# Performance work log

Hardware: AMD Instinct MI355X
Metric: run time of the kernel (lower is better)

The kernel has to match this reference:

```python
import jax, jax.numpy as jnp
import numpy as np

SCALE = 128.0          # GriddingDistance scale
GRID_MIN = -64.0       # floor(min coord) for points in (-64, 64)
R = 128                # voxels per axis = ceil(max) - floor(min)
G = R * R * R          # flattened grid size per sample

# 8 trilinear corner offsets (8, 3)
_CORNERS = jnp.array([[i, j, k] for i in (0, 1) for j in (0, 1) for k in (0, 1)], dtype=jnp.int32)


def _gridding(cloud):
    """Trilinear scatter of (b, n, 3) scaled points into (b, G) voxel grid.

    Mirrors gridding.forward: per point, weight each of the 8 surrounding
    voxel corners by prod(1 - |p - corner|) and scatter-add into the grid.
    """
    b, n, _ = cloud.shape
    p = cloud - GRID_MIN                     # shift to [0, R)
    x0f = jnp.floor(p)
    d = p - x0f                              # (b, n, 3) fractional offsets
    x0 = x0f.astype(jnp.int32)
    idx = jnp.clip(x0[:, :, None, :] + _CORNERS, 0, R - 1)      # (b, n, 8, 3)
    # corner weight: d for the +1 corner, (1 - d) for the base corner
    w = jnp.where(_CORNERS[None, None] == 1, d[:, :, None, :], 1.0 - d[:, :, None, :])
    w = w.prod(axis=-1)                      # (b, n, 8)
    flat = (idx[..., 0] * R + idx[..., 1]) * R + idx[..., 2]    # (b, n, 8)
    flat = flat + jnp.arange(b, dtype=jnp.int32)[:, None, None] * G
    grid = jnp.zeros(b * G, dtype=cloud.dtype).at[flat.reshape(-1)].add(w.reshape(-1))
    return grid.reshape(b, G)


def setup_inputs() -> dict:
    key = jax.random.key(0)
    k1, k2 = jax.random.split(key)
    # normalized clouds in (-0.49, 0.49) so scaled points stay inside the grid
    pred = (jax.random.uniform(k1, (8, 65536, 3), dtype=jnp.float32) - 0.5) * 0.98
    gt = (jax.random.uniform(k2, (8, 65536, 3), dtype=jnp.float32) - 0.5) * 0.98
    return {"pred_cloud": pred, "gt_cloud": gt}


def reference(pred_cloud, gt_cloud):
    pred_grid = _gridding(pred_cloud * SCALE)
    gt_grid = _gridding(gt_cloud * SCALE)
    return pred_grid, gt_grid
```

## Files before the change

### kernel.cpp

```cpp
#include <hip/hip_runtime.h>


#define RES   128
#define GRIDG (RES * RES * RES)
#define NSLAB 16
#define NREG  64
#define NBIN  (NSLAB * NREG)
#define CAPB  2048
#define PTS_PER_BLOCK 1024

__device__ __forceinline__ int clampi(int v) {
    return v < 0 ? 0 : (v > RES - 1 ? RES - 1 : v);
}


__global__ __launch_bounds__(256) void place_kernel(
    const float* __restrict__ pred, const float* __restrict__ gt,
    unsigned* __restrict__ cursor,
    float* __restrict__ bins,
    int npts, int nblkPerSlab)
{
    __shared__ unsigned cnt[NREG];
    __shared__ unsigned curs[NREG];

    const int gblk = blockIdx.x;
    const int slab = gblk / nblkPerSlab;
    const int blk  = gblk - slab * nblkPerSlab;
    const float* cloud = (slab < 8) ? pred : gt;
    const int sample = slab & 7;
    const float* cbase = cloud + (size_t)sample * npts * 3;

    if (threadIdx.x < NREG) cnt[threadIdx.x] = 0;
    __syncthreads();

    float px[4], py[4], pz[4];
    bool valid[4];

#pragma unroll
    for (int k = 0; k < 4; ++k) {
        const int j = blk * PTS_PER_BLOCK + k * 256 + threadIdx.x;
        valid[k] = (j < npts);
        if (valid[k]) {
            const float x = fmaf(cbase[(size_t)j * 3 + 0], 128.0f, 64.0f);
            const float y = fmaf(cbase[(size_t)j * 3 + 1], 128.0f, 64.0f);
            const float z = fmaf(cbase[(size_t)j * 3 + 2], 128.0f, 64.0f);
            px[k] = x; py[k] = y; pz[k] = z;
            const int ix = (int)floorf(x), iy = (int)floorf(y), iz = (int)floorf(z);
            const int rx0 = clampi(ix) >> 5, rx1 = clampi(ix + 1) >> 5;
            const int ry0 = clampi(iy) >> 5, ry1 = clampi(iy + 1) >> 5;
            const int rz0 = clampi(iz) >> 5, rz1 = clampi(iz + 1) >> 5;
            for (int a = rx0; a <= rx1; ++a)
                for (int b = ry0; b <= ry1; ++b)
                    for (int c = rz0; c <= rz1; ++c)
                        atomicAdd(&cnt[(a << 4) | (b << 2) | c], 1u);
        }
    }
    __syncthreads();

    if (threadIdx.x < NREG) {
        const unsigned c = cnt[threadIdx.x];
        unsigned base = 0;
        if (c) base = atomicAdd(&cursor[slab * NREG + threadIdx.x], c);
        curs[threadIdx.x] = base;
    }
    __syncthreads();

#pragma unroll
    for (int k = 0; k < 4; ++k) {
        if (!valid[k]) continue;
        const float x = px[k], y = py[k], z = pz[k];
        const int ix = (int)floorf(x), iy = (int)floorf(y), iz = (int)floorf(z);
        const int rx0 = clampi(ix) >> 5, rx1 = clampi(ix + 1) >> 5;
        const int ry0 = clampi(iy) >> 5, ry1 = clampi(iy + 1) >> 5;
        const int rz0 = clampi(iz) >> 5, rz1 = clampi(iz + 1) >> 5;
        for (int a = rx0; a <= rx1; ++a)
            for (int b = ry0; b <= ry1; ++b)
                for (int c = rz0; c <= rz1; ++c) {
                    const int r = (a << 4) | (b << 2) | c;
                    const unsigned slot = atomicAdd(&curs[r], 1u);
                    if (slot < CAPB) {
                        const size_t off = ((size_t)(slab * NREG + r) * CAPB + slot) * 3;
                        bins[off + 0] = x;
                        bins[off + 1] = y;
                        bins[off + 2] = z;
                    }
                }
    }
}

__global__ __launch_bounds__(1024) void accum_kernel(
    const float* __restrict__ bins, const unsigned* __restrict__ cursor,
    float* __restrict__ out)
{
    __shared__ __align__(16) float vox[32 * 32 * 32];

    const int bin  = blockIdx.x;
    const int slab = bin >> 6;
    const int reg  = bin & 63;
    const int rx = (reg >> 4) & 3, ry = (reg >> 2) & 3, rz = reg & 3;

    unsigned n = cursor[bin];
    if (n > CAPB) n = CAPB;

    for (int i = threadIdx.x; i < 32768; i += 1024) vox[i] = 0.0f;
    __syncthreads();

    const float* seg = bins + (size_t)bin * CAPB * 3;
    for (unsigned i = threadIdx.x; i < n; i += 1024) {
        const float x = seg[(size_t)i * 3 + 0];
        const float y = seg[(size_t)i * 3 + 1];
        const float z = seg[(size_t)i * 3 + 2];
        const float xf = floorf(x), yf = floorf(y), zf = floorf(z);
        const float dx = x - xf, dy = y - yf, dz = z - zf;
        const int ix = (int)xf, iy = (int)yf, iz = (int)zf;
        const int x0 = clampi(ix), x1 = clampi(ix + 1);
        const int y0 = clampi(iy), y1 = clampi(iy + 1);
        const int z0 = clampi(iz), z1 = clampi(iz + 1);
        const float wx0 = 1.0f - dx, wy0 = 1.0f - dy, wz0 = 1.0f - dz;

#pragma unroll
        for (int cc = 0; cc < 8; ++cc) {
            const int cx = (cc & 4) ? x1 : x0;
            const int cy = (cc & 2) ? y1 : y0;
            const int cz = (cc & 1) ? z1 : z0;
            if (((cx >> 5) == rx) & ((cy >> 5) == ry) & ((cz >> 5) == rz)) {
                const float w = ((cc & 4) ? dx : wx0) *
                                ((cc & 2) ? dy : wy0) *
                                ((cc & 1) ? dz : wz0);
                atomicAdd(&vox[((cx & 31) << 10) | ((cy & 31) << 5) | (cz & 31)], w);
            }
        }
    }
    __syncthreads();

    float* gp = out + (size_t)slab * GRIDG
              + ((size_t)rx << 19) + (ry << 12) + (rz << 5);
    for (int v = threadIdx.x; v < 8192; v += 1024) {
        const int l  = v << 2;
        const int lx = l >> 10, ly = (l >> 5) & 31, lz = l & 31;
        *(float4*)(gp + ((size_t)lx << 14) + (ly << 7) + lz) = *(const float4*)&vox[l];
    }
}


__global__ __launch_bounds__(256) void gridding_scatter_kernel(
    const float* __restrict__ cloud, float* __restrict__ grid, int n)
{
    const int j = blockIdx.x * blockDim.x + threadIdx.x;
    if (j >= n) return;
    const int b = blockIdx.y;
    const size_t pt = (size_t)b * n + j;

    const float x = fmaf(cloud[pt * 3 + 0], 128.0f, 64.0f);
    const float y = fmaf(cloud[pt * 3 + 1], 128.0f, 64.0f);
    const float z = fmaf(cloud[pt * 3 + 2], 128.0f, 64.0f);
    const float xf = floorf(x), yf = floorf(y), zf = floorf(z);
    const float dx = x - xf, dy = y - yf, dz = z - zf;
    const int ix = (int)xf, iy = (int)yf, iz = (int)zf;
    const int x0 = clampi(ix), x1 = clampi(ix + 1);
    const int y0 = clampi(iy), y1 = clampi(iy + 1);
    const int z0 = clampi(iz), z1 = clampi(iz + 1);
    const float wx0 = 1.0f - dx, wy0 = 1.0f - dy, wz0 = 1.0f - dz;

    float* gp = grid + (size_t)b * GRIDG;
    const int bx0 = x0 << 14, bx1 = x1 << 14;
    const int by0 = y0 << 7,  by1 = y1 << 7;
    atomicAdd(gp + (bx0 + by0 + z0), wx0 * wy0 * wz0);
    atomicAdd(gp + (bx0 + by0 + z1), wx0 * wy0 * dz);
    atomicAdd(gp + (bx0 + by1 + z0), wx0 * dy * wz0);
    atomicAdd(gp + (bx0 + by1 + z1), wx0 * dy * dz);
    atomicAdd(gp + (bx1 + by0 + z0), dx * wy0 * wz0);
    atomicAdd(gp + (bx1 + by0 + z1), dx * wy0 * dz);
    atomicAdd(gp + (bx1 + by1 + z0), dx * dy * wz0);
    atomicAdd(gp + (bx1 + by1 + z1), dx * dy * dz);
}


extern "C" void kernel_launch(void* const* d_in, const int* in_sizes, int n_in,
                              void* d_out, int out_size, void* d_ws, size_t ws_size,
                              hipStream_t stream) {
    const float* pred = (const float*)d_in[0];
    const float* gt   = (const float*)d_in[1];
    float* out = (float*)d_out;

    const int bsz  = 8;
    const int npts = in_sizes[0] / (bsz * 3);

    const size_t cursorBytes = 4096;
    const size_t binsBytes   = (size_t)NBIN * CAPB * 3 * sizeof(float);
    const size_t needWs      = cursorBytes + binsBytes;

    if (ws_size >= needWs) {
        unsigned* cursor = (unsigned*)d_ws;
        float* bins = (float*)((char*)d_ws + cursorBytes);

        hipMemsetAsync(cursor, 0, NBIN * sizeof(unsigned), stream);

        const int nblkPerSlab = (npts + PTS_PER_BLOCK - 1) / PTS_PER_BLOCK;
        place_kernel<<<dim3(NSLAB * nblkPerSlab), dim3(256), 0, stream>>>(
            pred, gt, cursor, bins, npts, nblkPerSlab);
        accum_kernel<<<dim3(NBIN), dim3(1024), 0, stream>>>(bins, cursor, out);
    } else {
        hipMemsetAsync(d_out, 0, (size_t)out_size * sizeof(float), stream);
        dim3 block(256);
        dim3 grid((npts + 255) / 256, bsz);
        float* pred_grid = out;
        float* gt_grid   = out + (size_t)bsz * GRIDG;
        gridding_scatter_kernel<<<grid, block, 0, stream>>>(pred, pred_grid, npts);
        gridding_scatter_kernel<<<grid, block, 0, stream>>>(gt,   gt_grid,   npts);
    }
}
```

Baseline: 192.9 us.

## Bin points into 16x16 xy columns with float4 records and vectorized loads

```diff
diff --git a/kernel.cpp b/kernel.cpp
--- a/kernel.cpp
+++ b/kernel.cpp
@@ -17,7 +17,7 @@
 __global__ __launch_bounds__(256) void place_kernel(
     const float* __restrict__ pred, const float* __restrict__ gt,
     unsigned* __restrict__ cursor,
-    float* __restrict__ bins,
+    float4* __restrict__ bins,
     int npts, int nblkPerSlab)
 {
     __shared__ unsigned cnt[NREG];
@@ -28,7 +28,7 @@
     const int blk  = gblk - slab * nblkPerSlab;
     const float* cloud = (slab < 8) ? pred : gt;
     const int sample = slab & 7;
-    const float* cbase = cloud + (size_t)sample * npts * 3;
+    const float* cbase = cloud + (size_t)sample * npts * 3 + (size_t)blk * PTS_PER_BLOCK * 3;
 
     if (threadIdx.x < NREG) cnt[threadIdx.x] = 0;
     __syncthreads();
@@ -36,24 +36,49 @@
     float px[4], py[4], pz[4];
     bool valid[4];
 
+    const int t = threadIdx.x;
+    const bool fullBlock = ((blk + 1) * PTS_PER_BLOCK) <= npts;
+
+    if (fullBlock) {
+        const float4* b4 = (const float4*)cbase;
+        const float4 f0 = b4[3 * t + 0];
+        const float4 f1 = b4[3 * t + 1];
+        const float4 f2 = b4[3 * t + 2];
+        px[0] = f0.x; py[0] = f0.y; pz[0] = f0.z;
+        px[1] = f0.w; py[1] = f1.x; pz[1] = f1.y;
+        px[2] = f1.z; py[2] = f1.w; pz[2] = f2.x;
+        px[3] = f2.y; py[3] = f2.z; pz[3] = f2.w;
+#pragma unroll
+        for (int k = 0; k < 4; ++k) {
+            valid[k] = true;
+            px[k] = fmaf(px[k], 128.0f, 64.0f);
+            py[k] = fmaf(py[k], 128.0f, 64.0f);
+            pz[k] = fmaf(pz[k], 128.0f, 64.0f);
+        }
+    } else {
+#pragma unroll
+        for (int k = 0; k < 4; ++k) {
+            const int j = blk * PTS_PER_BLOCK + 4 * t + k;
+            const int jj = 4 * t + k;
+            valid[k] = (blk * PTS_PER_BLOCK + jj < npts);
+            if (valid[k]) {
+                px[k] = fmaf(cbase[(size_t)jj * 3 + 0], 128.0f, 64.0f);
+                py[k] = fmaf(cbase[(size_t)jj * 3 + 1], 128.0f, 64.0f);
+                pz[k] = fmaf(cbase[(size_t)jj * 3 + 2], 128.0f, 64.0f);
+            }
+            (void)j;
+        }
+    }
+
 #pragma unroll
     for (int k = 0; k < 4; ++k) {
-        const int j = blk * PTS_PER_BLOCK + k * 256 + threadIdx.x;
-        valid[k] = (j < npts);
-        if (valid[k]) {
-            const float x = fmaf(cbase[(size_t)j * 3 + 0], 128.0f, 64.0f);
-            const float y = fmaf(cbase[(size_t)j * 3 + 1], 128.0f, 64.0f);
-            const float z = fmaf(cbase[(size_t)j * 3 + 2], 128.0f, 64.0f);
-            px[k] = x; py[k] = y; pz[k] = z;
-            const int ix = (int)floorf(x), iy = (int)floorf(y), iz = (int)floorf(z);
-            const int rx0 = clampi(ix) >> 5, rx1 = clampi(ix + 1) >> 5;
-            const int ry0 = clampi(iy) >> 5, ry1 = clampi(iy + 1) >> 5;
-            const int rz0 = clampi(iz) >> 5, rz1 = clampi(iz + 1) >> 5;
-            for (int a = rx0; a <= rx1; ++a)
-                for (int b = ry0; b <= ry1; ++b)
-                    for (int c = rz0; c <= rz1; ++c)
-                        atomicAdd(&cnt[(a << 4) | (b << 2) | c], 1u);
-        }
+        if (!valid[k]) continue;
+        const int ix = (int)floorf(px[k]), iy = (int)floorf(py[k]);
+        const int rx0 = clampi(ix) >> 4, rx1 = clampi(ix + 1) >> 4;
+        const int ry0 = clampi(iy) >> 4, ry1 = clampi(iy + 1) >> 4;
+        for (int a = rx0; a <= rx1; ++a)
+            for (int b = ry0; b <= ry1; ++b)
+                atomicAdd(&cnt[(a << 3) | b], 1u);
     }
     __syncthreads();
 
@@ -69,47 +94,43 @@
     for (int k = 0; k < 4; ++k) {
         if (!valid[k]) continue;
         const float x = px[k], y = py[k], z = pz[k];
-        const int ix = (int)floorf(x), iy = (int)floorf(y), iz = (int)floorf(z);
-        const int rx0 = clampi(ix) >> 5, rx1 = clampi(ix + 1) >> 5;
-        const int ry0 = clampi(iy) >> 5, ry1 = clampi(iy + 1) >> 5;
-        const int rz0 = clampi(iz) >> 5, rz1 = clampi(iz + 1) >> 5;
+        const int ix = (int)floorf(x), iy = (int)floorf(y);
+        const int rx0 = clampi(ix) >> 4, rx1 = clampi(ix + 1) >> 4;
+        const int ry0 = clampi(iy) >> 4, ry1 = clampi(iy + 1) >> 4;
         for (int a = rx0; a <= rx1; ++a)
-            for (int b = ry0; b <= ry1; ++b)
-                for (int c = rz0; c <= rz1; ++c) {
-                    const int r = (a << 4) | (b << 2) | c;
-                    const unsigned slot = atomicAdd(&curs[r], 1u);
-                    if (slot < CAPB) {
-                        const size_t off = ((size_t)(slab * NREG + r) * CAPB + slot) * 3;
-                        bins[off + 0] = x;
-                        bins[off + 1] = y;
-                        bins[off + 2] = z;
-                    }
+            for (int b = ry0; b <= ry1; ++b) {
+                const int r = (a << 3) | b;
+                const unsigned slot = atomicAdd(&curs[r], 1u);
+                if (slot < CAPB) {
+                    bins[(size_t)(slab * NREG + r) * CAPB + slot] =
+                        make_float4(x, y, z, 0.0f);
                 }
+            }
     }
 }
 
 __global__ __launch_bounds__(1024) void accum_kernel(
-    const float* __restrict__ bins, const unsigned* __restrict__ cursor,
+    const float4* __restrict__ bins, const unsigned* __restrict__ cursor,
     float* __restrict__ out)
 {
-    __shared__ __align__(16) float vox[32 * 32 * 32];
+    __shared__ __align__(16) float vox[16 * 16 * 128];
 
     const int bin  = blockIdx.x;
     const int slab = bin >> 6;
     const int reg  = bin & 63;
-    const int rx = (reg >> 4) & 3, ry = (reg >> 2) & 3, rz = reg & 3;
+    const int rx = reg >> 3, ry = reg & 7;
 
     unsigned n = cursor[bin];
     if (n > CAPB) n = CAPB;
 
-    for (int i = threadIdx.x; i < 32768; i += 1024) vox[i] = 0.0f;
-    __syncthreads();
-
-    const float* seg = bins + (size_t)bin * CAPB * 3;
+    float4* v4 = (float4*)vox;
+    for (int i = threadIdx.x; i < 8192; i += 1024) v4[i] = make_float4(0, 0, 0, 0);
+    __syncthreads();
+
+    const float4* seg = bins + (size_t)bin * CAPB;
     for (unsigned i = threadIdx.x; i < n; i += 1024) {
-        const float x = seg[(size_t)i * 3 + 0];
-        const float y = seg[(size_t)i * 3 + 1];
-        const float z = seg[(size_t)i * 3 + 2];
+        const float4 e = seg[i];
+        const float x = e.x, y = e.y, z = e.z;
         const float xf = floorf(x), yf = floorf(y), zf = floorf(z);
         const float dx = x - xf, dy = y - yf, dz = z - zf;
         const int ix = (int)xf, iy = (int)yf, iz = (int)zf;
@@ -119,26 +140,29 @@
         const float wx0 = 1.0f - dx, wy0 = 1.0f - dy, wz0 = 1.0f - dz;
 
 #pragma unroll
-        for (int cc = 0; cc < 8; ++cc) {
-            const int cx = (cc & 4) ? x1 : x0;
-            const int cy = (cc & 2) ? y1 : y0;
-            const int cz = (cc & 1) ? z1 : z0;
-            if (((cx >> 5) == rx) & ((cy >> 5) == ry) & ((cz >> 5) == rz)) {
-                const float w = ((cc & 4) ? dx : wx0) *
-                                ((cc & 2) ? dy : wy0) *
-                                ((cc & 1) ? dz : wz0);
-                atomicAdd(&vox[((cx & 31) << 10) | ((cy & 31) << 5) | (cz & 31)], w);
+        for (int sx = 0; sx < 2; ++sx) {
+            const int cx = sx ? x1 : x0;
+            if ((cx >> 4) != rx) continue;
+            const float wx = sx ? dx : wx0;
+#pragma unroll
+            for (int sy = 0; sy < 2; ++sy) {
+                const int cy = sy ? y1 : y0;
+                if ((cy >> 4) != ry) continue;
+                const float wxy = wx * (sy ? dy : wy0);
+                const int base = ((cx & 15) << 11) | ((cy & 15) << 7);
+                atomicAdd(&vox[base + z0], wxy * wz0);
+                atomicAdd(&vox[base + z1], wxy * dz);
             }
         }
     }
     __syncthreads();
 
-    float* gp = out + (size_t)slab * GRIDG
-              + ((size_t)rx << 19) + (ry << 12) + (rz << 5);
+    float* gp = out + (size_t)slab * GRIDG + ((size_t)rx << 18) + ((size_t)ry << 11);
     for (int v = threadIdx.x; v < 8192; v += 1024) {
         const int l  = v << 2;
-        const int lx = l >> 10, ly = (l >> 5) & 31, lz = l & 31;
-        *(float4*)(gp + ((size_t)lx << 14) + (ly << 7) + lz) = *(const float4*)&vox[l];
+        const int lx = l >> 11;
+        const int rem = l & 2047;
+        *(float4*)(gp + ((size_t)lx << 14) + rem) = v4[v];
     }
 }
 
@@ -187,12 +211,12 @@
     const int npts = in_sizes[0] / (bsz * 3);
 
     const size_t cursorBytes = 4096;
-    const size_t binsBytes   = (size_t)NBIN * CAPB * 3 * sizeof(float);
+    const size_t binsBytes   = (size_t)NBIN * CAPB * sizeof(float4);
     const size_t needWs      = cursorBytes + binsBytes;
 
     if (ws_size >= needWs) {
         unsigned* cursor = (unsigned*)d_ws;
-        float* bins = (float*)((char*)d_ws + cursorBytes);
+        float4* bins = (float4*)((char*)d_ws + cursorBytes);
 
         hipMemsetAsync(cursor, 0, NBIN * sizeof(unsigned), stream);
 
```

After: 190.6 us. About the same (-1.2%).
